# Optimization experiments

Measured on AMD Instinct MI355X. Metric: run time of the kernel, lower is better.

Reference implementation:

```python
import jax, jax.numpy as jnp
import numpy as np

B = 1048576   # batch of samples
L = 81        # leaf classes (hardcoded in the module)
G = 9         # synthetic 2-level hierarchy: 9 groups of 9 leaves under one root


def setup_inputs() -> dict:
    key = jax.random.key(0)
    k1, k2 = jax.random.split(key)
    outputs = jax.random.normal(k1, (B, L), dtype=jnp.float32)
    target = jax.random.randint(k2, (B,), 0, L, dtype=jnp.int32)
    return {"outputs": outputs, "target": target}


def reference(outputs, target):
    sft = jax.nn.softmax(outputs, axis=1)                 # [B, 81] leaf probs
    gp = sft.reshape(-1, G, G).sum(-1)                    # [B, 9] internal-node probs (sum of descendant leaves)
    parent = target // G                                  # [B] parent group of each target leaf
    p_parent = jnp.take_along_axis(gp, parent[:, None], axis=1)[:, 0]
    p_leaf = jnp.take_along_axis(sft, target[:, None], axis=1)[:, 0]
    win = 0.5 * p_parent + 0.5 * p_leaf
    loss = -jnp.log(win).mean()
    # greedy top-down argmax prediction: best group, then best leaf within that group
    g = jnp.argmax(gp, axis=1)                            # [B]
    within = jnp.take_along_axis(sft.reshape(-1, G, G), g[:, None, None], axis=1)[:, 0, :]  # [B, 9]
    pred = g * G + jnp.argmax(within, axis=1)             # [B]
    # synchronized walk to common ancestor: leaves at equal depth -> dist in {0,1,2}
    same_group = (pred // G) == parent
    total_dist = jnp.where(pred == target, 0, jnp.where(same_group, 1, 2)).sum()
    return loss, pred, total_dist
```

## Files before the change

kernel.cpp:

```cpp
#include <hip/hip_runtime.h>
#include <cstdint>

constexpr int BTOT  = 1048576;
constexpr int LCLS  = 81;
constexpr int GRP   = 9;
constexpr int ROWS  = 128;
constexpr int THR   = 64;
constexpr int NBLK  = BTOT / ROWS;
constexpr int TILEF = ROWS * LCLS;
constexpr int TILE4 = TILEF / 4;
constexpr int FULLR = TILE4 / THR;
constexpr int TAIL  = TILE4 - FULLR * THR;
constexpr float FIX = 67108864.0f;

__device__ __forceinline__ void gload_lds16(const float* gsrc, float* ldst) {
    __builtin_amdgcn_global_load_lds(
        (const __attribute__((address_space(1))) void*)gsrc,
        (__attribute__((address_space(3))) void*)ldst,
        16, 0, 0);
}

__device__ __attribute__((noinline)) int refine_group_f64(const float* __restrict__ xrow)
{
    double best = -1.0; int bi = 0;
    #pragma unroll
    for (int g = 0; g < GRP; ++g) {
        double s = 0.0;
        #pragma unroll
        for (int j = 0; j < GRP; ++j) s += exp((double)xrow[g * GRP + j]);
        if (s > best) { best = s; bi = g; }
    }
    return bi;
}

__device__ __forceinline__ void do_row(
    const float* __restrict__ xr,
    const float* __restrict__ xg,
    int t, float* __restrict__ outp,
    unsigned long long& lq, unsigned& dT)
{
    float gs[GRP];
    #pragma unroll
    for (int g = 0; g < GRP; ++g) {
        float s = 0.0f;
        #pragma unroll
        for (int j = 0; j < GRP; ++j) s += __expf(xr[g * GRP + j]);
        gs[g] = s;
    }
    float S = gs[0];
    #pragma unroll
    for (int g = 1; g < GRP; ++g) S += gs[g];

    float g1 = gs[0], g2 = -1e30f; int gi = 0;
    #pragma unroll
    for (int g = 1; g < GRP; ++g) {
        const float v = gs[g];
        const bool gt2 = v > g1;
        g2 = gt2 ? g1 : (v > g2 ? v : g2);
        g1 = gt2 ? v  : g1;
        gi = gt2 ? g  : gi;
    }

    const int parent = t / GRP;
    float gpar = gs[0];
    #pragma unroll
    for (int g = 1; g < GRP; ++g)
        gpar = (parent == g) ? gs[g] : gpar;

    if (g1 - g2 < 1e-5f * g1) gi = refine_group_f64(xg);

    const int wb = gi * GRP;
    float w1 = xr[wb]; int wi = 0;
    #pragma unroll
    for (int j = 1; j < GRP; ++j) {
        const float v = xr[wb + j];
        if (v > w1) { w1 = v; wi = j; }
    }
    const int pred = gi * GRP + wi;

    const float et  = expf(xr[t]);
    const float win = 0.5f * (gpar + et) / S;
    const float nl  = -logf(win);
    lq += (unsigned long long)llrintf(nl * FIX);
    dT += (pred == t) ? 0u : ((gi == parent) ? 1u : 2u);

    *outp = (float)pred;
}

__global__ __launch_bounds__(THR) void hl_main(
    const float* __restrict__ x, const int* __restrict__ tgt,
    float* __restrict__ out, unsigned long long* __restrict__ part)
{
    __shared__ float tile[TILEF];
    const int lane = threadIdx.x;
    const int blk  = blockIdx.x;
    const size_t tbase = (size_t)blk * TILEF;
    const float* gt = x + tbase;

    const int rowA = blk * ROWS + lane;
    const int rowB = rowA + 64;
    const int tA = tgt[rowA];
    const int tB = tgt[rowB];

    #pragma unroll
    for (int r = 0; r < FULLR; ++r) {
        const int i = r * THR + lane;
        gload_lds16(gt + 4 * i, &tile[4 * i]);
    }
    if (lane < TAIL) {
        const int i = FULLR * THR + lane;
        gload_lds16(gt + 4 * i, &tile[4 * i]);
    }

    unsigned long long lq = 0;
    unsigned dT = 0;

    asm volatile("s_waitcnt vmcnt(20)" ::: "memory");
    __builtin_amdgcn_sched_barrier(0);
    do_row(tile + lane * LCLS, x + tbase + (size_t)lane * LCLS,
           tA, out + 1 + rowA, lq, dT);

    asm volatile("s_waitcnt vmcnt(1)" ::: "memory");
    __builtin_amdgcn_sched_barrier(0);
    do_row(tile + (64 + lane) * LCLS, x + tbase + (size_t)(64 + lane) * LCLS,
           tB, out + 1 + rowB, lq, dT);

    #pragma unroll
    for (int off = 32; off > 0; off >>= 1) {
        lq += __shfl_down(lq, off);
        dT += __shfl_down(dT, off);
    }
    if (lane == 0) {
        part[blk] = lq;
        part[NBLK + blk] = (unsigned long long)dT;
    }
}

__global__ __launch_bounds__(1024) void hl_final(
    const unsigned long long* __restrict__ part, float* __restrict__ out)
{
    const int tid = threadIdx.x;
    unsigned long long a = 0, b = 0;
    for (int i = tid; i < NBLK; i += 1024) { a += part[i]; b += part[NBLK + i]; }
    #pragma unroll
    for (int off = 32; off > 0; off >>= 1) { a += __shfl_down(a, off); b += __shfl_down(b, off); }
    __shared__ unsigned long long rA[16], rB[16];
    if ((tid & 63) == 0) { rA[tid >> 6] = a; rB[tid >> 6] = b; }
    __syncthreads();
    if (tid == 0) {
        unsigned long long ta = 0, tb = 0;
        #pragma unroll
        for (int w = 0; w < 16; ++w) { ta += rA[w]; tb += rB[w]; }
        const double loss = ((double)ta / 67108864.0) / (double)BTOT;
        out[0] = (float)loss;
        out[1 + BTOT] = (float)tb;
    }
}

extern "C" void kernel_launch(void* const* d_in, const int* in_sizes, int n_in,
                              void* d_out, int out_size, void* d_ws, size_t ws_size,
                              hipStream_t stream) {
    const float* outputs = (const float*)d_in[0];
    const int*   target  = (const int*)d_in[1];
    float* out = (float*)d_out;
    unsigned long long* part = (unsigned long long*)d_ws;

    hl_main<<<NBLK, THR, 0, stream>>>(outputs, target, out, part);
    hl_final<<<1, 1024, 0, stream>>>(part, out);
}
```

Baseline: 80.02 us.

## Shrink per-block rows, narrow partial sums, and parallelize final reduction with atomics

Each block now handles 32 rows instead of 128, so there are four times as many blocks and only half the lanes of each wave do row work. Per-block partials shrink to 32-bit loss and 16-bit distance at a lower fixed-point scale. The final reduction runs across 8 blocks combined with atomics and a ticket counter, which adds a memset launch. The aim is more parallelism and less reduction traffic, at the cost of idle lanes, lower fixed-point precision and possible 32-bit overflow of the per-block loss sum.

After: 81.00 us. Within noise of the previous version (+1.2%).

```diff
diff --git a/kernel.cpp b/kernel.cpp
--- a/kernel.cpp
+++ b/kernel.cpp
@@ -4,14 +4,14 @@
 constexpr int BTOT  = 1048576;
 constexpr int LCLS  = 81;
 constexpr int GRP   = 9;
-constexpr int ROWS  = 128;
+constexpr int ROWS  = 32;
 constexpr int THR   = 64;
 constexpr int NBLK  = BTOT / ROWS;
 constexpr int TILEF = ROWS * LCLS;
 constexpr int TILE4 = TILEF / 4;
 constexpr int FULLR = TILE4 / THR;
 constexpr int TAIL  = TILE4 - FULLR * THR;
-constexpr float FIX = 67108864.0f;
+constexpr float FIX = 1048576.0f;
 
 __device__ __forceinline__ void gload_lds16(const float* gsrc, float* ldst) {
     __builtin_amdgcn_global_load_lds(
@@ -34,10 +34,8 @@
 }
 
 __device__ __forceinline__ void do_row(
-    const float* __restrict__ xr,
-    const float* __restrict__ xg,
-    int t, float* __restrict__ outp,
-    unsigned long long& lq, unsigned& dT)
+    const float* __restrict__ xr, const float* __restrict__ xg,
+    int t, float* __restrict__ outp, unsigned& lq, unsigned& dT)
 {
     float gs[GRP];
     #pragma unroll
@@ -81,7 +79,7 @@
     const float et  = expf(xr[t]);
     const float win = 0.5f * (gpar + et) / S;
     const float nl  = -logf(win);
-    lq += (unsigned long long)llrintf(nl * FIX);
+    lq += (unsigned)lrintf(nl * FIX);
     dT += (pred == t) ? 0u : ((gi == parent) ? 1u : 2u);
 
     *outp = (float)pred;
@@ -89,7 +87,8 @@
 
 __global__ __launch_bounds__(THR) void hl_main(
     const float* __restrict__ x, const int* __restrict__ tgt,
-    float* __restrict__ out, unsigned long long* __restrict__ part)
+    float* __restrict__ out,
+    unsigned* __restrict__ partL, unsigned short* __restrict__ partD)
 {
     __shared__ float tile[TILEF];
     const int lane = threadIdx.x;
@@ -97,10 +96,8 @@
     const size_t tbase = (size_t)blk * TILEF;
     const float* gt = x + tbase;
 
-    const int rowA = blk * ROWS + lane;
-    const int rowB = rowA + 64;
-    const int tA = tgt[rowA];
-    const int tB = tgt[rowB];
+    int t = 0;
+    if (lane < ROWS) t = tgt[blk * ROWS + lane];
 
     #pragma unroll
     for (int r = 0; r < FULLR; ++r) {
@@ -112,18 +109,14 @@
         gload_lds16(gt + 4 * i, &tile[4 * i]);
     }
 
-    unsigned long long lq = 0;
-    unsigned dT = 0;
+    asm volatile("s_waitcnt vmcnt(0)" ::: "memory");
+    __builtin_amdgcn_sched_barrier(0);
 
-    asm volatile("s_waitcnt vmcnt(20)" ::: "memory");
-    __builtin_amdgcn_sched_barrier(0);
-    do_row(tile + lane * LCLS, x + tbase + (size_t)lane * LCLS,
-           tA, out + 1 + rowA, lq, dT);
-
-    asm volatile("s_waitcnt vmcnt(1)" ::: "memory");
-    __builtin_amdgcn_sched_barrier(0);
-    do_row(tile + (64 + lane) * LCLS, x + tbase + (size_t)(64 + lane) * LCLS,
-           tB, out + 1 + rowB, lq, dT);
+    unsigned lq = 0, dT = 0;
+    if (lane < ROWS) {
+        do_row(tile + lane * LCLS, x + tbase + (size_t)lane * LCLS,
+               t, out + 1 + blk * ROWS + lane, lq, dT);
+    }
 
     #pragma unroll
     for (int off = 32; off > 0; off >>= 1) {
@@ -131,29 +124,40 @@
         dT += __shfl_down(dT, off);
     }
     if (lane == 0) {
-        part[blk] = lq;
-        part[NBLK + blk] = (unsigned long long)dT;
+        partL[blk] = lq;
+        partD[blk] = (unsigned short)dT;
     }
 }
 
 __global__ __launch_bounds__(1024) void hl_final(
-    const unsigned long long* __restrict__ part, float* __restrict__ out)
+    const unsigned* __restrict__ partL, const unsigned short* __restrict__ partD,
+    unsigned long long* __restrict__ acc, float* __restrict__ out)
 {
-    const int tid = threadIdx.x;
+    const int idx = blockIdx.x * 1024 + threadIdx.x;
     unsigned long long a = 0, b = 0;
-    for (int i = tid; i < NBLK; i += 1024) { a += part[i]; b += part[NBLK + i]; }
+    for (int i = idx; i < NBLK; i += 8 * 1024) { a += partL[i]; b += partD[i]; }
     #pragma unroll
     for (int off = 32; off > 0; off >>= 1) { a += __shfl_down(a, off); b += __shfl_down(b, off); }
     __shared__ unsigned long long rA[16], rB[16];
+    const int tid = threadIdx.x;
     if ((tid & 63) == 0) { rA[tid >> 6] = a; rB[tid >> 6] = b; }
     __syncthreads();
     if (tid == 0) {
         unsigned long long ta = 0, tb = 0;
         #pragma unroll
         for (int w = 0; w < 16; ++w) { ta += rA[w]; tb += rB[w]; }
-        const double loss = ((double)ta / 67108864.0) / (double)BTOT;
-        out[0] = (float)loss;
-        out[1 + BTOT] = (float)tb;
+        atomicAdd(&acc[0], ta);
+        atomicAdd(&acc[1], tb);
+        __threadfence();
+        unsigned* tick = (unsigned*)(acc + 2);
+        const unsigned old = atomicAdd(tick, 1u);
+        if (old == 7u) {
+            __threadfence();
+            const unsigned long long fa = atomicAdd(&acc[0], 0ull);
+            const unsigned long long fb = atomicAdd(&acc[1], 0ull);
+            out[0] = (float)(((double)fa / 1048576.0) / (double)BTOT);
+            out[1 + BTOT] = (float)fb;
+        }
     }
 }
 
@@ -163,8 +167,12 @@
     const float* outputs = (const float*)d_in[0];
     const int*   target  = (const int*)d_in[1];
     float* out = (float*)d_out;
-    unsigned long long* part = (unsigned long long*)d_ws;
 
-    hl_main<<<NBLK, THR, 0, stream>>>(outputs, target, out, part);
-    hl_final<<<1, 1024, 0, stream>>>(part, out);
+    unsigned*       partL = (unsigned*)d_ws;
+    unsigned short* partD = (unsigned short*)((char*)d_ws + 131072);
+    unsigned long long* acc = (unsigned long long*)((char*)d_ws + 196608);
+
+    hipMemsetAsync((char*)d_ws + 196608, 0, 24, stream);
+    hl_main<<<NBLK, THR, 0, stream>>>(outputs, target, out, partL, partD);
+    hl_final<<<8, 1024, 0, stream>>>(partL, partD, acc, out);
 }
```
